# Kernel optimization log

Hardware: AMD Instinct MI355X
Metric: run time of the kernel (lower is better)

Reference implementation:

```python
import jax, jax.numpy as jnp
import numpy as np


def _sparse_mask(T, S, W, G):
    """Replicates CustomSparseAttention._create_sparse_mask (bool [T, S])."""
    ii = np.arange(T)[:, None]
    jj = np.arange(S)[None, :]
    # local sliding window: cols in [i - W//2, i + W//2]
    m = (jj >= ii - W // 2) & (jj <= ii + W // 2)
    # overlapping block windows every (W - W//4) rows
    ov = W // 4
    for i in range(0, T, W - ov):
        m[i:i + W, max(0, i - ov):min(S, i + W + ov)] = True
    # strided global tokens
    if G > 0:
        stride = S // (G + 1)
        gi = np.linspace(stride, S - stride, G).astype(np.int64)  # torch .long() truncates
        m[:, gi] = True
    # diagonal +/- 1
    m |= np.abs(jj - ii) <= 1
    return jnp.asarray(m)


def setup_inputs() -> dict:
    key = jax.random.key(0)
    ks = jax.random.split(key, 8)
    B, T, S, E = 2, 2048, 2048, 512
    std = 0.02
    return {
        "query": jax.random.normal(ks[0], (B, T, E), jnp.float32),
        "key": jax.random.normal(ks[1], (B, S, E), jnp.float32),
        "value": jax.random.normal(ks[2], (B, S, E), jnp.float32),
        "Wq": jax.random.normal(ks[3], (E, E), jnp.float32) * std,
        "bq": jnp.zeros((E,), jnp.float32),
        "Wk": jax.random.normal(ks[4], (E, E), jnp.float32) * std,
        "bk": jnp.zeros((E,), jnp.float32),
        "Wv": jax.random.normal(ks[5], (E, E), jnp.float32) * std,
        "bv": jnp.zeros((E,), jnp.float32),
        "Wo": jax.random.normal(ks[6], (E, E), jnp.float32) * std,
        "bo": jnp.zeros((E,), jnp.float32),
        "temperature": jnp.ones((1,), jnp.float32) * 0.1,
        "local_window_size": 128,
        "num_global_tokens": 16,
    }


def reference(query, key, value, Wq, bq, Wk, bk, Wv, bv, Wo, bo,
              temperature, local_window_size, num_global_tokens):
    B, T, E = query.shape
    S = key.shape[1]
    H = 16
    hd = E // H
    scaling = float(hd) ** -0.5

    q = (query @ Wq.T + bq) * scaling          # [B, T, E]
    k = key @ Wk.T + bk                        # [B, S, E]
    v = value @ Wv.T + bv                      # [B, S, E]

    q = q.reshape(B, T, H, hd)
    k = k.reshape(B, S, H, hd)
    v = v.reshape(B, S, H, hd)

    # [B, H, T, S] dense scores, scaled by learned temperature
    attn = jnp.einsum('bthd,bshd->bhts', q, k) * temperature[0]

    mask = _sparse_mask(T, S, local_window_size, num_global_tokens)  # [T, S] bool
    attn = jnp.where(mask[None, None], attn, -jnp.inf)

    # (row-max subtraction in the original is the standard stable softmax)
    attn = jax.nn.softmax(attn, axis=-1)

    out = jnp.einsum('bhts,bshd->bthd', attn, v).reshape(B, T, E)
    out = out @ Wo.T + bo
    return out
```

## Files before the change

kernel.cpp:

```cpp
#include <hip/hip_runtime.h>

typedef _Float16 f16x8 __attribute__((ext_vector_type(8)));
typedef float f32x4 __attribute__((ext_vector_type(4)));

#define Tt 2048
#define Ee 512
#define Hh 16
#define HD 32
#define Bb 2
#define Mm (Bb*Tt)

__device__ __constant__ int GCOLS[16] = {120,240,361,481,602,722,843,963,
                                         1084,1204,1325,1445,1566,1686,1807,1928};

__device__ __forceinline__ int lo_of(int i) {
    int kmin = (i >= 32) ? ((i - 32) / 96) : 0;
    int lo = kmin * 96 - 32;
    return lo < 0 ? 0 : lo;
}
__device__ __forceinline__ int hi_of(int i) {
    int hi = (i / 96) * 96 + 160;
    return hi > Tt ? Tt : hi;
}

__device__ __forceinline__ f16x8 cvt8(float4 a, float4 b) {
    f16x8 r;
    r[0]=(_Float16)a.x; r[1]=(_Float16)a.y; r[2]=(_Float16)a.z; r[3]=(_Float16)a.w;
    r[4]=(_Float16)b.x; r[5]=(_Float16)b.y; r[6]=(_Float16)b.z; r[7]=(_Float16)b.w;
    return r;
}

__global__ __launch_bounds__(256)
void proj_kernel(const float* __restrict__ query, const float* __restrict__ key_,
                 const float* __restrict__ value,
                 const float* __restrict__ Wq, const float* __restrict__ bq,
                 const float* __restrict__ Wk, const float* __restrict__ bk,
                 const float* __restrict__ Wv, const float* __restrict__ bv,
                 const float* __restrict__ temp,
                 _Float16* __restrict__ q_ws, _Float16* __restrict__ k_ws,
                 _Float16* __restrict__ v_ws)
{
    const int z = blockIdx.z;
    const float* A    = (z==0)? query : (z==1)? key_ : value;
    const float* Wm   = (z==0)? Wq    : (z==1)? Wk   : Wv;
    const float* bias = (z==0)? bq    : (z==1)? bk   : bv;

    const int m0 = blockIdx.x * 128;
    const int n0 = blockIdx.y * 64;

    __shared__ _Float16 Ash[128*40];
    __shared__ _Float16 Bsh[64*40];

    const int tid  = threadIdx.x;
    const int lane = tid & 63, wave = tid >> 6;
    const int quad = lane >> 4, l16 = lane & 15;
    const int wm = wave >> 1, wn = wave & 1;

    const int arow = tid >> 1, akoff = (tid & 1) * 16;
    const int brow = tid >> 2, bkoff = (tid & 3) * 8;

    f32x4 acc[4][2] = {};

    for (int k0 = 0; k0 < Ee; k0 += 32) {
        const float* ap = A + (size_t)(m0 + arow) * Ee + k0 + akoff;
        float4 a0 = ((const float4*)ap)[0];
        float4 a1 = ((const float4*)ap)[1];
        float4 a2 = ((const float4*)ap)[2];
        float4 a3 = ((const float4*)ap)[3];
        const float* bp = Wm + (size_t)(n0 + brow) * Ee + k0 + bkoff;
        float4 b0 = ((const float4*)bp)[0];
        float4 b1 = ((const float4*)bp)[1];

        __syncthreads();
        *(f16x8*)&Ash[arow*40 + akoff    ] = cvt8(a0, a1);
        *(f16x8*)&Ash[arow*40 + akoff + 8] = cvt8(a2, a3);
        *(f16x8*)&Bsh[brow*40 + bkoff    ] = cvt8(b0, b1);
        __syncthreads();

        f16x8 af[4], bf[2];
        #pragma unroll
        for (int mt = 0; mt < 4; mt++)
            af[mt] = *(const f16x8*)&Ash[(wm*64 + mt*16 + l16)*40 + quad*8];
        #pragma unroll
        for (int nt = 0; nt < 2; nt++)
            bf[nt] = *(const f16x8*)&Bsh[(wn*32 + nt*16 + l16)*40 + quad*8];
        #pragma unroll
        for (int mt = 0; mt < 4; mt++)
            #pragma unroll
            for (int nt = 0; nt < 2; nt++)
                acc[mt][nt] = __builtin_amdgcn_mfma_f32_16x16x32_f16(af[mt], bf[nt], acc[mt][nt], 0, 0, 0);
    }

    const float scale = (z == 0) ? (0.17677669529663687f * temp[0]) : 1.0f;
    #pragma unroll
    for (int nt = 0; nt < 2; nt++) {
        const int n = n0 + wn*32 + nt*16 + l16;
        const float bn = bias[n];
        const int h = n >> 5, d = n & 31;
        #pragma unroll
        for (int mt = 0; mt < 4; mt++) {
            #pragma unroll
            for (int r = 0; r < 4; r++) {
                const int m = m0 + wm*64 + mt*16 + quad*4 + r;
                const float val = (acc[mt][nt][r] + bn) * scale;
                const int bidx = m >> 11, t = m & (Tt - 1);
                if (z == 2) {
                    v_ws[((size_t)(bidx*Hh + h)*HD + d)*Tt + t] = (_Float16)val;
                } else {
                    _Float16* dst = (z == 0) ? q_ws : k_ws;
                    dst[((size_t)(bidx*Hh + h)*Tt + t)*HD + d] = (_Float16)val;
                }
            }
        }
    }
}

__global__ __launch_bounds__(256)
void attn_kernel(const _Float16* __restrict__ q_ws, const _Float16* __restrict__ k_ws,
                 const _Float16* __restrict__ v_ws, _Float16* __restrict__ o_ws)
{
    const int qb = blockIdx.x * 64;
    const int h  = blockIdx.y;
    const int b  = blockIdx.z;
    const int bh = b * Hh + h;

    const int tid  = threadIdx.x;
    const int lane = tid & 63, wave = tid >> 6;
    const int quad = lane >> 4, l16 = lane & 15;
    const int t0   = qb + wave * 16;

    __shared__ _Float16 P_lds[4][16*72];
    _Float16* myP = &P_lds[wave][0];

    const f16x8 qf = *(const f16x8*)(q_ws + ((size_t)bh*Tt + t0 + l16)*HD + quad*8);

    int lo[4], hi[4];
    #pragma unroll
    for (int r = 0; r < 4; r++) {
        const int i = t0 + quad*4 + r;
        lo[r] = lo_of(i); hi[r] = hi_of(i);
    }

    float lsum[4] = {0.f, 0.f, 0.f, 0.f};
    f32x4 accO[2] = {};
    const f32x4 zf = {0.f, 0.f, 0.f, 0.f};

    {
        const int gj = GCOLS[l16];
        const f16x8 kg = *(const f16x8*)(k_ws + ((size_t)bh*Tt + gj)*HD + quad*8);
        const f32x4 s = __builtin_amdgcn_mfma_f32_16x16x32_f16(qf, kg, zf, 0, 0, 0);
        #pragma unroll
        for (int r = 0; r < 4; r++) {
            const bool inside = (gj >= lo[r]) & (gj < hi[r]);
            const float p = inside ? 0.f : __expf(s[r]);
            const _Float16 ph = (_Float16)p;
            lsum[r] += (float)ph;
            myP[(quad*4 + r)*72 + l16] = ph;
        }
        f16x8 pf;
        if (quad < 2) pf = *(const f16x8*)&myP[l16*72 + quad*8];
        else {
            #pragma unroll
            for (int j = 0; j < 8; j++) pf[j] = (_Float16)0.f;
        }
        int gck[8];
        #pragma unroll
        for (int j = 0; j < 8; j++) gck[j] = (quad < 2) ? GCOLS[quad*8 + j] : 0;
        #pragma unroll
        for (int dt = 0; dt < 2; dt++) {
            f16x8 vg;
            if (quad < 2) {
                const _Float16* vrow = v_ws + ((size_t)bh*HD + dt*16 + l16)*Tt;
                #pragma unroll
                for (int j = 0; j < 8; j++) vg[j] = vrow[gck[j]];
            } else {
                #pragma unroll
                for (int j = 0; j < 8; j++) vg[j] = (_Float16)0.f;
            }
            accO[dt] = __builtin_amdgcn_mfma_f32_16x16x32_f16(pf, vg, accO[dt], 0, 0, 0);
        }
    }

    const int cstart = lo_of(qb) & ~63;
    const int cend   = hi_of(qb + 63);
    for (int j0 = cstart; j0 < cend; j0 += 64) {
        f16x8 kf[4]; f32x4 s[4];
        #pragma unroll
        for (int nt = 0; nt < 4; nt++)
            kf[nt] = *(const f16x8*)(k_ws + ((size_t)bh*Tt + j0 + nt*16 + l16)*HD + quad*8);
        #pragma unroll
        for (int nt = 0; nt < 4; nt++)
            s[nt] = __builtin_amdgcn_mfma_f32_16x16x32_f16(qf, kf[nt], zf, 0, 0, 0);
        #pragma unroll
        for (int nt = 0; nt < 4; nt++) {
            const int j = j0 + nt*16 + l16;
            #pragma unroll
            for (int r = 0; r < 4; r++) {
                const bool inside = (j >= lo[r]) & (j < hi[r]);
                const float p = inside ? __expf(s[nt][r]) : 0.f;
                const _Float16 ph = (_Float16)p;
                lsum[r] += (float)ph;
                myP[(quad*4 + r)*72 + nt*16 + l16] = ph;
            }
        }
        #pragma unroll
        for (int kt = 0; kt < 2; kt++) {
            const f16x8 pf = *(const f16x8*)&myP[l16*72 + kt*32 + quad*8];
            #pragma unroll
            for (int dt = 0; dt < 2; dt++) {
                const f16x8 vf = *(const f16x8*)(v_ws + ((size_t)bh*HD + dt*16 + l16)*Tt
                                                 + j0 + kt*32 + quad*8);
                accO[dt] = __builtin_amdgcn_mfma_f32_16x16x32_f16(pf, vf, accO[dt], 0, 0, 0);
            }
        }
    }

    #pragma unroll
    for (int r = 0; r < 4; r++) {
        float v = lsum[r];
        v += __shfl_xor(v, 1);
        v += __shfl_xor(v, 2);
        v += __shfl_xor(v, 4);
        v += __shfl_xor(v, 8);
        lsum[r] = 1.0f / v;
    }
    #pragma unroll
    for (int dt = 0; dt < 2; dt++) {
        #pragma unroll
        for (int r = 0; r < 4; r++) {
            const int t = t0 + quad*4 + r;
            const int d = dt*16 + l16;
            o_ws[((size_t)(b*Tt + t)*Hh + h)*HD + d] = (_Float16)(accO[dt][r] * lsum[r]);
        }
    }
}

__global__ __launch_bounds__(256)
void out_kernel(const _Float16* __restrict__ Aw, const float* __restrict__ Wo,
                const float* __restrict__ bo, float* __restrict__ out)
{
    const int m0 = blockIdx.x * 128;
    const int n0 = blockIdx.y * 64;

    __shared__ _Float16 Ash[128*40];
    __shared__ _Float16 Bsh[64*40];

    const int tid  = threadIdx.x;
    const int lane = tid & 63, wave = tid >> 6;
    const int quad = lane >> 4, l16 = lane & 15;
    const int wm = wave >> 1, wn = wave & 1;

    const int arow = tid >> 1, akoff = (tid & 1) * 16;
    const int brow = tid >> 2, bkoff = (tid & 3) * 8;

    f32x4 acc[4][2] = {};

    for (int k0 = 0; k0 < Ee; k0 += 32) {
        const _Float16* ap = Aw + (size_t)(m0 + arow) * Ee + k0 + akoff;
        const f16x8 av0 = ((const f16x8*)ap)[0];
        const f16x8 av1 = ((const f16x8*)ap)[1];
        const float* bp = Wo + (size_t)(n0 + brow) * Ee + k0 + bkoff;
        float4 b0 = ((const float4*)bp)[0];
        float4 b1 = ((const float4*)bp)[1];

        __syncthreads();
        *(f16x8*)&Ash[arow*40 + akoff    ] = av0;
        *(f16x8*)&Ash[arow*40 + akoff + 8] = av1;
        *(f16x8*)&Bsh[brow*40 + bkoff    ] = cvt8(b0, b1);
        __syncthreads();

        f16x8 af[4], bf[2];
        #pragma unroll
        for (int mt = 0; mt < 4; mt++)
            af[mt] = *(const f16x8*)&Ash[(wm*64 + mt*16 + l16)*40 + quad*8];
        #pragma unroll
        for (int nt = 0; nt < 2; nt++)
            bf[nt] = *(const f16x8*)&Bsh[(wn*32 + nt*16 + l16)*40 + quad*8];
        #pragma unroll
        for (int mt = 0; mt < 4; mt++)
            #pragma unroll
            for (int nt = 0; nt < 2; nt++)
                acc[mt][nt] = __builtin_amdgcn_mfma_f32_16x16x32_f16(af[mt], bf[nt], acc[mt][nt], 0, 0, 0);
    }

    #pragma unroll
    for (int nt = 0; nt < 2; nt++) {
        const int n = n0 + wn*32 + nt*16 + l16;
        const float bn = bo[n];
        #pragma unroll
        for (int mt = 0; mt < 4; mt++) {
            #pragma unroll
            for (int r = 0; r < 4; r++) {
                const int m = m0 + wm*64 + mt*16 + quad*4 + r;
                out[(size_t)m * Ee + n] = acc[mt][nt][r] + bn;
            }
        }
    }
}

extern "C" void kernel_launch(void* const* d_in, const int* in_sizes, int n_in,
                              void* d_out, int out_size, void* d_ws, size_t ws_size,
                              hipStream_t stream)
{
    const float* query = (const float*)d_in[0];
    const float* key_  = (const float*)d_in[1];
    const float* value = (const float*)d_in[2];
    const float* Wq    = (const float*)d_in[3];
    const float* bq    = (const float*)d_in[4];
    const float* Wk    = (const float*)d_in[5];
    const float* bk    = (const float*)d_in[6];
    const float* Wv    = (const float*)d_in[7];
    const float* bv    = (const float*)d_in[8];
    const float* Wo    = (const float*)d_in[9];
    const float* bo    = (const float*)d_in[10];
    const float* temp  = (const float*)d_in[11];

    _Float16* q_ws = (_Float16*)d_ws;
    _Float16* k_ws = q_ws + (size_t)Mm * Ee;
    _Float16* v_ws = k_ws + (size_t)Mm * Ee;
    _Float16* o_ws = v_ws + (size_t)Mm * Ee;
    float* out = (float*)d_out;

    proj_kernel<<<dim3(32, 8, 3), 256, 0, stream>>>(query, key_, value,
                                                    Wq, bq, Wk, bk, Wv, bv, temp,
                                                    q_ws, k_ws, v_ws);
    attn_kernel<<<dim3(32, 16, 2), 256, 0, stream>>>(q_ws, k_ws, v_ws, o_ws);
    out_kernel<<<dim3(32, 8, 1), 256, 0, stream>>>(o_ws, Wo, bo, out);
}
```

Before: 151.4 us.

## Pre-convert inputs and weights to fp16, use direct global-to-LDS loads in GEMMs

```diff
diff --git a/kernel.cpp b/kernel.cpp
--- a/kernel.cpp
+++ b/kernel.cpp
@@ -30,85 +30,113 @@
     return r;
 }
 
+__device__ __forceinline__ void async_copy16(const _Float16* g, _Float16* l) {
+    __builtin_amdgcn_global_load_lds(
+        (const __attribute__((address_space(1))) void*)g,
+        (__attribute__((address_space(3))) void*)l, 16, 0, 0);
+}
+
 __global__ __launch_bounds__(256)
-void proj_kernel(const float* __restrict__ query, const float* __restrict__ key_,
-                 const float* __restrict__ value,
-                 const float* __restrict__ Wq, const float* __restrict__ bq,
-                 const float* __restrict__ Wk, const float* __restrict__ bk,
-                 const float* __restrict__ Wv, const float* __restrict__ bv,
-                 const float* __restrict__ temp,
+void cvt_kernel(const float* __restrict__ q, const float* __restrict__ k,
+                const float* __restrict__ v,
+                const float* __restrict__ wq, const float* __restrict__ wk,
+                const float* __restrict__ wv, const float* __restrict__ wo,
+                _Float16* __restrict__ dst)
+{
+    const int g8 = blockIdx.x * 256 + threadIdx.x;
+    const float* src;
+    if (g8 < 786432) {
+        const int s = g8 >> 18;
+        const float* xs = (s == 0) ? q : (s == 1) ? k : v;
+        src = xs + (size_t)(g8 & 262143) * 8;
+    } else {
+        const int w8 = g8 - 786432;
+        const int s = w8 >> 15;
+        const float* ws = (s == 0) ? wq : (s == 1) ? wk : (s == 2) ? wv : wo;
+        src = ws + (size_t)(w8 & 32767) * 8;
+    }
+    float4 a = ((const float4*)src)[0];
+    float4 b = ((const float4*)src)[1];
+    *(f16x8*)(dst + (size_t)g8 * 8) = cvt8(a, b);
+}
+
+__global__ __launch_bounds__(256)
+void proj_kernel(const _Float16* __restrict__ xw,
+                 const float* __restrict__ bq, const float* __restrict__ bk,
+                 const float* __restrict__ bv, const float* __restrict__ temp,
                  _Float16* __restrict__ q_ws, _Float16* __restrict__ k_ws,
                  _Float16* __restrict__ v_ws)
 {
     const int z = blockIdx.z;
-    const float* A    = (z==0)? query : (z==1)? key_ : value;
-    const float* Wm   = (z==0)? Wq    : (z==1)? Wk   : Wv;
-    const float* bias = (z==0)? bq    : (z==1)? bk   : bv;
-
-    const int m0 = blockIdx.x * 128;
-    const int n0 = blockIdx.y * 64;
-
-    __shared__ _Float16 Ash[128*40];
-    __shared__ _Float16 Bsh[64*40];
+    const _Float16* A = xw + (size_t)z * (Mm * Ee);
+    const _Float16* W = xw + (size_t)3 * Mm * Ee + (size_t)z * (Ee * Ee);
+    const float* bias = (z == 0) ? bq : (z == 1) ? bk : bv;
+
+    const int m0 = blockIdx.x * 64;
+    const int n0 = blockIdx.y * 128;
+
+    __shared__ _Float16 Ash[64 * 32];
+    __shared__ _Float16 Bsh[128 * 32];
 
     const int tid  = threadIdx.x;
     const int lane = tid & 63, wave = tid >> 6;
     const int quad = lane >> 4, l16 = lane & 15;
-    const int wm = wave >> 1, wn = wave & 1;
-
-    const int arow = tid >> 1, akoff = (tid & 1) * 16;
-    const int brow = tid >> 2, bkoff = (tid & 3) * 8;
-
-    f32x4 acc[4][2] = {};
+    const int wm = wave & 1, wn = wave >> 1;
+
+    const int arow = tid >> 2;
+    const int ac   = (tid & 3) ^ ((arow >> 1) & 3);
+    const _Float16* agp  = A + (size_t)(m0 + arow) * Ee + ac * 8;
+    const _Float16* bgp0 = W + (size_t)(n0 + arow) * Ee + ac * 8;
+    const _Float16* bgp1 = W + (size_t)(n0 + 64 + arow) * Ee + ac * 8;
+    _Float16* AshW  = Ash + wave * 512;
+    _Float16* BshW0 = Bsh + wave * 512;
+    _Float16* BshW1 = Bsh + 2048 + wave * 512;
+
+    f32x4 acc[2][4] = {};
 
     for (int k0 = 0; k0 < Ee; k0 += 32) {
-        const float* ap = A + (size_t)(m0 + arow) * Ee + k0 + akoff;
-        float4 a0 = ((const float4*)ap)[0];
-        float4 a1 = ((const float4*)ap)[1];
-        float4 a2 = ((const float4*)ap)[2];
-        float4 a3 = ((const float4*)ap)[3];
-        const float* bp = Wm + (size_t)(n0 + brow) * Ee + k0 + bkoff;
-        float4 b0 = ((const float4*)bp)[0];
-        float4 b1 = ((const float4*)bp)[1];
-
         __syncthreads();
-        *(f16x8*)&Ash[arow*40 + akoff    ] = cvt8(a0, a1);
-        *(f16x8*)&Ash[arow*40 + akoff + 8] = cvt8(a2, a3);
-        *(f16x8*)&Bsh[brow*40 + bkoff    ] = cvt8(b0, b1);
+        async_copy16(agp + k0, AshW);
+        async_copy16(bgp0 + k0, BshW0);
+        async_copy16(bgp1 + k0, BshW1);
         __syncthreads();
 
-        f16x8 af[4], bf[2];
-        #pragma unroll
-        for (int mt = 0; mt < 4; mt++)
-            af[mt] = *(const f16x8*)&Ash[(wm*64 + mt*16 + l16)*40 + quad*8];
-        #pragma unroll
-        for (int nt = 0; nt < 2; nt++)
-            bf[nt] = *(const f16x8*)&Bsh[(wn*32 + nt*16 + l16)*40 + quad*8];
-        #pragma unroll
-        for (int mt = 0; mt < 4; mt++)
-            #pragma unroll
-            for (int nt = 0; nt < 2; nt++)
+        f16x8 af[2], bf[4];
+        #pragma unroll
+        for (int mt = 0; mt < 2; mt++) {
+            const int row = wm * 32 + mt * 16 + l16;
+            af[mt] = *(const f16x8*)&Ash[row * 32 + ((quad ^ ((row >> 1) & 3)) * 8)];
+        }
+        #pragma unroll
+        for (int nt = 0; nt < 4; nt++) {
+            const int row = wn * 64 + nt * 16 + l16;
+            bf[nt] = *(const f16x8*)&Bsh[row * 32 + ((quad ^ ((row >> 1) & 3)) * 8)];
+        }
+        #pragma unroll
+        for (int mt = 0; mt < 2; mt++)
+            #pragma unroll
+            for (int nt = 0; nt < 4; nt++)
                 acc[mt][nt] = __builtin_amdgcn_mfma_f32_16x16x32_f16(af[mt], bf[nt], acc[mt][nt], 0, 0, 0);
     }
 
     const float scale = (z == 0) ? (0.17677669529663687f * temp[0]) : 1.0f;
     #pragma unroll
-    for (int nt = 0; nt < 2; nt++) {
-        const int n = n0 + wn*32 + nt*16 + l16;
+    for (int nt = 0; nt < 4; nt++) {
+        const int n = n0 + wn * 64 + nt * 16 + l16;
         const float bn = bias[n];
         const int h = n >> 5, d = n & 31;
         #pragma unroll
-        for (int mt = 0; mt < 4; mt++) {
+        for (int mt = 0; mt < 2; mt++) {
             #pragma unroll
             for (int r = 0; r < 4; r++) {
-                const int m = m0 + wm*64 + mt*16 + quad*4 + r;
+                const int m = m0 + wm * 32 + mt * 16 + quad * 4 + r;
                 const float val = (acc[mt][nt][r] + bn) * scale;
                 const int bidx = m >> 11, t = m & (Tt - 1);
                 if (z == 2) {
-                    v_ws[((size_t)(bidx*Hh + h)*HD + d)*Tt + t] = (_Float16)val;
+                    v_ws[((size_t)(bidx * Hh + h) * HD + d) * Tt + t] = (_Float16)val;
                 } else {
                     _Float16* dst = (z == 0) ? q_ws : k_ws;
-                    dst[((size_t)(bidx*Hh + h)*Tt + t)*HD + d] = (_Float16)val;
+                    dst[((size_t)(bidx * Hh + h) * Tt + t) * HD + d] = (_Float16)val;
                 }
             }
         }
@@ -236,62 +264,65 @@
 }
 
 __global__ __launch_bounds__(256)
-void out_kernel(const _Float16* __restrict__ Aw, const float* __restrict__ Wo,
+void out_kernel(const _Float16* __restrict__ Aw, const _Float16* __restrict__ Wof,
                 const float* __restrict__ bo, float* __restrict__ out)
 {
-    const int m0 = blockIdx.x * 128;
-    const int n0 = blockIdx.y * 64;
-
-    __shared__ _Float16 Ash[128*40];
-    __shared__ _Float16 Bsh[64*40];
+    const int m0 = blockIdx.x * 64;
+    const int n0 = blockIdx.y * 128;
+
+    __shared__ _Float16 Ash[64 * 32];
+    __shared__ _Float16 Bsh[128 * 32];
 
     const int tid  = threadIdx.x;
     const int lane = tid & 63, wave = tid >> 6;
     const int quad = lane >> 4, l16 = lane & 15;
-    const int wm = wave >> 1, wn = wave & 1;
-
-    const int arow = tid >> 1, akoff = (tid & 1) * 16;
-    const int brow = tid >> 2, bkoff = (tid & 3) * 8;
-
-    f32x4 acc[4][2] = {};
+    const int wm = wave & 1, wn = wave >> 1;
+
+    const int arow = tid >> 2;
+    const int ac   = (tid & 3) ^ ((arow >> 1) & 3);
+    const _Float16* agp  = Aw  + (size_t)(m0 + arow) * Ee + ac * 8;
+    const _Float16* bgp0 = Wof + (size_t)(n0 + arow) * Ee + ac * 8;
+    const _Float16* bgp1 = Wof + (size_t)(n0 + 64 + arow) * Ee + ac * 8;
+    _Float16* AshW  = Ash + wave * 512;
+    _Float16* BshW0 = Bsh + wave * 512;
+    _Float16* BshW1 = Bsh + 2048 + wave * 512;
+
+    f32x4 acc[2][4] = {};
 
     for (int k0 = 0; k0 < Ee; k0 += 32) {
-        const _Float16* ap = Aw + (size_t)(m0 + arow) * Ee + k0 + akoff;
-        const f16x8 av0 = ((const f16x8*)ap)[0];
-        const f16x8 av1 = ((const f16x8*)ap)[1];
-        const float* bp = Wo + (size_t)(n0 + brow) * Ee + k0 + bkoff;
-        float4 b0 = ((const float4*)bp)[0];
-        float4 b1 = ((const float4*)bp)[1];
-
         __syncthreads();
-        *(f16x8*)&Ash[arow*40 + akoff    ] = av0;
-        *(f16x8*)&Ash[arow*40 + akoff + 8] = av1;
-        *(f16x8*)&Bsh[brow*40 + bkoff    ] = cvt8(b0, b1);
+        async_copy16(agp + k0, AshW);
+        async_copy16(bgp0 + k0, BshW0);
+        async_copy16(bgp1 + k0, BshW1);
         __syncthreads();
 
-        f16x8 af[4], bf[2];
-        #pragma unroll
-        for (int mt = 0; mt < 4; mt++)
-            af[mt] = *(const f16x8*)&Ash[(wm*64 + mt*16 + l16)*40 + quad*8];
-        #pragma unroll
-        for (int nt = 0; nt < 2; nt++)
-            bf[nt] = *(const f16x8*)&Bsh[(wn*32 + nt*16 + l16)*40 + quad*8];
-        #pragma unroll
-        for (int mt = 0; mt < 4; mt++)
-            #pragma unroll
-            for (int nt = 0; nt < 2; nt++)
+        f16x8 af[2], bf[4];
+        #pragma unroll
+        for (int mt = 0; mt < 2; mt++) {
+            const int row = wm * 32 + mt * 16 + l16;
+            af[mt] = *(const f16x8*)&Ash[row * 32 + ((quad ^ ((row >> 1) & 3)) * 8)];
+        }
+        #pragma unroll
+        for (int nt = 0; nt < 4; nt++) {
+            const int row = wn * 64 + nt * 16 + l16;
+            bf[nt] = *(const f16x8*)&Bsh[row * 32 + ((quad ^ ((row >> 1) & 3)) * 8)];
+        }
+        #pragma unroll
+        for (int mt = 0; mt < 2; mt++)
+            #pragma unroll
+            for (int nt = 0; nt < 4; nt++)
                 acc[mt][nt] = __builtin_amdgcn_mfma_f32_16x16x32_f16(af[mt], bf[nt], acc[mt][nt], 0, 0, 0);
     }
 
     #pragma unroll
-    for (int nt = 0; nt < 2; nt++) {
-        const int n = n0 + wn*32 + nt*16 + l16;
+    for (int nt = 0; nt < 4; nt++) {
+        const int n = n0 + wn * 64 + nt * 16 + l16;
         const float bn = bo[n];
         #pragma unroll
-        for (int mt = 0; mt < 4; mt++) {
+        for (int mt = 0; mt < 2; mt++) {
             #pragma unroll
             for (int r = 0; r < 4; r++) {
-                const int m = m0 + wm*64 + mt*16 + quad*4 + r;
+                const int m = m0 + wm * 32 + mt * 16 + quad * 4 + r;
                 out[(size_t)m * Ee + n] = acc[mt][nt][r] + bn;
             }
         }
@@ -315,15 +346,17 @@
     const float* bo    = (const float*)d_in[10];
     const float* temp  = (const float*)d_in[11];
 
-    _Float16* q_ws = (_Float16*)d_ws;
+    _Float16* xw   = (_Float16*)d_ws;
+    _Float16* q_ws = xw + 7340032;
     _Float16* k_ws = q_ws + (size_t)Mm * Ee;
     _Float16* v_ws = k_ws + (size_t)Mm * Ee;
     _Float16* o_ws = v_ws + (size_t)Mm * Ee;
+    const _Float16* Wof = xw + (size_t)3 * Mm * Ee + (size_t)3 * Ee * Ee;
     float* out = (float*)d_out;
 
-    proj_kernel<<<dim3(32, 8, 3), 256, 0, stream>>>(query, key_, value,
-                                                    Wq, bq, Wk, bk, Wv, bv, temp,
+    cvt_kernel<<<3584, 256, 0, stream>>>(query, key_, value, Wq, Wk, Wv, Wo, xw);
+    proj_kernel<<<dim3(64, 4, 3), 256, 0, stream>>>(xw, bq, bk, bv, temp,
                                                     q_ws, k_ws, v_ws);
     attn_kernel<<<dim3(32, 16, 2), 256, 0, stream>>>(q_ws, k_ws, v_ws, o_ws);
-    out_kernel<<<dim3(32, 8, 1), 256, 0, stream>>>(o_ws, Wo, bo, out);
-}
+    out_kernel<<<dim3(64, 4), 256, 0, stream>>>(o_ws, Wof, bo, out);
+}
```

Measured after the change: 149.8 us. Within noise of the previous version (-1.1%).
